# Optimization experiments

Measured on AMD Instinct MI355X. Metric: run time of the kernel, lower is better.

Reference implementation:

```python
import jax, jax.numpy as jnp
import numpy as np

NUM_ITERS = 3

def squash(s, axis=-1):
    # standard capsule squash: ||s||^2/(1+||s||^2) * s/||s||
    sq = jnp.sum(s * s, axis=axis, keepdims=True)
    norm = jnp.sqrt(sq)
    return (sq / (1.0 + sq)) * (s / norm)

def setup_inputs() -> dict:
    key = jax.random.key(0)
    kx, kw = jax.random.split(key)
    B, I, k, l, O = 512, 1152, 8, 16, 7
    x = jax.random.normal(kx, (B, I, k), dtype=jnp.float32)
    w = jax.random.normal(kw, (I, k, l, O), dtype=jnp.float32)
    return {"x": x, "w": w}

def reference(x, w):
    # x: [B, I, k]; w: [I, k, l, O]
    u_hat = jnp.einsum('BIk,IklO->BIlO', x, w)            # [B, I, l, O]
    I, _, l, _ = w.shape
    b_ij = jnp.zeros((I, l), dtype=u_hat.dtype)
    v_j = None
    for _ in range(NUM_ITERS):
        c_ij = jax.nn.softmax(b_ij, axis=0)               # softmax over I
        s_j = jnp.einsum('Il,BIlO->BlO', c_ij, u_hat)     # [B, l, O]
        v_j = jnp.transpose(squash(s_j), (0, 2, 1))       # [B, O, l]
        u_vj = jnp.einsum('BOl,BIlO->BIl', v_j, u_hat).mean(axis=0)  # [I, l]
        b_ij = b_ij + u_vj
    return v_j
```

## Files before the change

### kernel.cpp

```cpp
#include <hip/hip_runtime.h>
#include <hip/hip_bf16.h>


#define NB 512
#define NI 1152
#define NLO 112
#define NIK 9216
#define KSPLIT 96
#define SPART 57344

typedef __attribute__((ext_vector_type(8))) short bf16x8;
typedef __attribute__((ext_vector_type(4))) float f32x4;

__device__ __forceinline__ ushort f2bf(float f) {
    __hip_bfloat16 h = __float2bfloat16(f);
    return *(ushort*)&h;
}

__device__ __forceinline__ void conv_x_body(const float* __restrict__ x,
                                            ushort* __restrict__ xbf,
                                            ushort* __restrict__ xT, int bid) {
    __shared__ ushort tile[64][68];
    int kg = bid % 144, bg = bid / 144;
    int k0 = kg * 64, b0 = bg * 64;
    int t = threadIdx.x;
    for (int e = t; e < 1024; e += 256) {
        int r = e >> 4, c4 = (e & 15) * 4;
        float4 f = *(const float4*)&x[(size_t)(b0 + r) * NIK + k0 + c4];
        ushort4 u = { f2bf(f.x), f2bf(f.y), f2bf(f.z), f2bf(f.w) };
        *(ushort4*)&xbf[(size_t)(b0 + r) * NIK + k0 + c4] = u;
        tile[r][c4] = u.x; tile[r][c4 + 1] = u.y; tile[r][c4 + 2] = u.z; tile[r][c4 + 3] = u.w;
    }
    __syncthreads();
    for (int e = t; e < 1024; e += 256) {
        int kr = e >> 4, c4 = (e & 15) * 4;
        ushort4 u = { tile[c4][kr], tile[c4 + 1][kr], tile[c4 + 2][kr], tile[c4 + 3][kr] };
        *(ushort4*)&xT[(size_t)(k0 + kr) * NB + b0 + c4] = u;
    }
}

__device__ __forceinline__ void wc_tile(const float* __restrict__ cs_sh,
                                        const float* __restrict__ w,
                                        ushort* __restrict__ wcT, int ik0) {
    __shared__ ushort tile[NLO][66];
    int t = threadIdx.x;
    for (int e = t; e < 7168; e += 256) {
        int ikl = e / NLO, lo = e - ikl * NLO;
        int il = ((ikl >> 3) << 4) + lo / 7;
        tile[lo][ikl] = f2bf(cs_sh[il] * w[(size_t)(ik0 + ikl) * NLO + lo]);
    }
    __syncthreads();
    for (int e = t; e < 7168; e += 256) {
        int lo = e >> 6, ikl = e & 63;
        wcT[(size_t)lo * NIK + ik0 + ikl] = tile[lo][ikl];
    }
}

__global__ __launch_bounds__(256) void prep0(const float* __restrict__ x,
                                             ushort* __restrict__ xbf,
                                             ushort* __restrict__ xT,
                                             const float* __restrict__ w,
                                             ushort* __restrict__ wcT,
                                             float* __restrict__ Z) {
    if (blockIdx.x < 1152) { conv_x_body(x, xbf, xT, blockIdx.x); return; }
    __shared__ float cs[128];
    int t = threadIdx.x;
    if (blockIdx.x == 1152 && t < 48) Z[t] = (t < 16) ? 1.0f : 0.0f;
    if (t < 128) cs[t] = 1.0f / 1152.0f;
    __syncthreads();
    wc_tile(cs, w, wcT, (blockIdx.x - 1152) * 64);
}

__global__ __launch_bounds__(256) void wc_exp(const float* __restrict__ bijp,
                                              const float* __restrict__ w,
                                              ushort* __restrict__ wcT,
                                              float* __restrict__ Zit) {
    __shared__ float cs[128];
    int ik0 = blockIdx.x * 64;
    int t = threadIdx.x;
    if (t < 128) {
        int e = (ik0 >> 3) * 16 + t;
        cs[t] = expf(bijp[e] + bijp[e + NI * 16]);
    }
    __syncthreads();
    if (t < 16) {
        float z = 0.f;
        #pragma unroll
        for (int j = 0; j < 8; ++j) z += cs[j * 16 + t];
        atomicAdd(&Zit[t], z);
    }
    wc_tile(cs, w, wcT, ik0);
}

__global__ __launch_bounds__(256) void s_gemm(const ushort* __restrict__ xbf,
                                              const ushort* __restrict__ wcT,
                                              float* __restrict__ part) {
    int wid = blockIdx.x * 4 + (threadIdx.x >> 6);
    int lane = threadIdx.x & 63;
    int mt = wid & 31;
    int kc = wid >> 5;
    int b0 = mt * 16, k0 = kc * 96;
    int row = lane & 15, quad = lane >> 4;
    const ushort* ap = xbf + (size_t)(b0 + row) * NIK + k0 + quad * 8;
    const ushort* bp = wcT + (size_t)row * NIK + k0 + quad * 8;
    f32x4 acc[7];
    #pragma unroll
    for (int nt = 0; nt < 7; ++nt) acc[nt] = (f32x4){0.f, 0.f, 0.f, 0.f};
    #pragma unroll
    for (int ks = 0; ks < 3; ++ks) {
        bf16x8 a = *(const bf16x8*)(ap + ks * 32);
        #pragma unroll
        for (int nt = 0; nt < 7; ++nt) {
            bf16x8 bfr = *(const bf16x8*)(bp + (size_t)nt * 16 * NIK + ks * 32);
            acc[nt] = __builtin_amdgcn_mfma_f32_16x16x32_bf16(a, bfr, acc[nt], 0, 0, 0);
        }
    }
    float* pp = part + (size_t)kc * SPART + (size_t)(b0 + quad * 4) * NLO + row;
    #pragma unroll
    for (int nt = 0; nt < 7; ++nt)
        #pragma unroll
        for (int r = 0; r < 4; ++r)
            pp[(size_t)r * NLO + nt * 16] = acc[nt][r];
}

__global__ void squash_k(const float* __restrict__ part, ushort* __restrict__ vT,
                         float* __restrict__ out, const float* __restrict__ Zit,
                         int write_out) {
    int b = blockIdx.x;
    int t = threadIdx.x;
    __shared__ float sh[NLO];
    __shared__ float fac[16];
    __shared__ float zinv[16];
    if (t >= 112 && t < 128) zinv[t - 112] = 1.0f / Zit[t - 112];
    float sv = 0.f;
    if (t < NLO) {
        const float* p = part + (size_t)b * NLO + t;
        #pragma unroll 8
        for (int kc = 0; kc < KSPLIT; ++kc) sv += p[(size_t)kc * SPART];
    }
    __syncthreads();
    if (t < NLO) { sv *= zinv[t / 7]; sh[t] = sv; }
    __syncthreads();
    if (t < 16) {
        float sq = 0.f;
        #pragma unroll
        for (int o = 0; o < 7; ++o) { float e = sh[t * 7 + o]; sq += e * e; }
        fac[t] = sqrtf(sq) / (1.0f + sq);
    }
    __syncthreads();
    if (t < NLO) {
        int l = t / 7, o = t - l * 7;
        float vv = sv * fac[l];
        vT[(size_t)(o * 16 + l) * NB + b] = f2bf(vv);
        if (write_out) out[(size_t)b * NLO + o * 16 + l] = vv;
    }
}

__global__ __launch_bounds__(256) void g_fused(const ushort* __restrict__ xT,
                                               const ushort* __restrict__ vT,
                                               const float* __restrict__ w,
                                               float* __restrict__ bijp, int accum) {
    int wid = blockIdx.x * 4 + (threadIdx.x >> 6);
    int lane = threadIdx.x & 63;
    int half = wid & 1;
    int m0 = (wid >> 1) * 16;
    int kb0 = half * 256;
    int row = lane & 15, quad = lane >> 4;
    const ushort* ap = xT + (size_t)(m0 + row) * NB + kb0 + quad * 8;
    const ushort* bp = vT + (size_t)row * NB + kb0 + quad * 8;
    f32x4 acc[7];
    #pragma unroll
    for (int nt = 0; nt < 7; ++nt) acc[nt] = (f32x4){0.f, 0.f, 0.f, 0.f};
    #pragma unroll
    for (int ks = 0; ks < 8; ++ks) {
        bf16x8 a = *(const bf16x8*)(ap + ks * 32);
        #pragma unroll
        for (int nt = 0; nt < 7; ++nt) {
            bf16x8 bfr = *(const bf16x8*)(bp + (size_t)nt * 16 * NB + ks * 32);
            acc[nt] = __builtin_amdgcn_mfma_f32_16x16x32_bf16(a, bfr, acc[nt], 0, 0, 0);
        }
    }
    float S = 0.f;
    #pragma unroll
    for (int r = 0; r < 4; ++r) {
        int ik = m0 + quad * 4 + r;
        const float* wr = w + (size_t)ik * NLO + row * 7;
        float p = 0.f;
        #pragma unroll
        for (int o = 0; o < 7; ++o) p += wr[o] * acc[o][r];
        S += p;
    }
    float Sp = __shfl_down(S, 16);
    if ((quad & 1) == 0) {
        int i = (m0 >> 3) + (quad >> 1);
        float val = (S + Sp) * (1.0f / 512.0f);
        float* dst = bijp + (size_t)half * (NI * 16) + i * 16 + row;
        *dst = accum ? (*dst + val) : val;
    }
}

extern "C" void kernel_launch(void* const* d_in, const int* in_sizes, int n_in,
                              void* d_out, int out_size, void* d_ws, size_t ws_size,
                              hipStream_t stream) {
    const float* x = (const float*)d_in[0];
    const float* w = (const float*)d_in[1];
    float* out = (float*)d_out;
    float* ws = (float*)d_ws;
    float*  f_bijp = ws;
    float*  f_Z    = f_bijp + 2 * NI * 16;
    float*  f_part = f_Z + 48;
    ushort* xbf    = (ushort*)(f_part + (size_t)KSPLIT * SPART);
    ushort* xT     = xbf + (size_t)NB * NIK;
    ushort* wcT    = xT + (size_t)NIK * NB;
    ushort* vT     = wcT + (size_t)NLO * NIK;
    prep0<<<1296, 256, 0, stream>>>(x, xbf, xT, w, wcT, f_Z);
    for (int it = 0; it < 3; ++it) {
        if (it > 0) wc_exp<<<144, 256, 0, stream>>>(f_bijp, w, wcT, f_Z + it * 16);
        s_gemm<<<768, 256, 0, stream>>>(xbf, wcT, f_part);
        squash_k<<<512, 128, 0, stream>>>(f_part, vT, out, f_Z + it * 16,
                                          it == 2 ? 1 : 0);
        if (it < 2) g_fused<<<288, 256, 0, stream>>>(xT, vT, w, f_bijp, it);
    }
}
```

Before: 185.9 us.

## Fuse routing-logit update with softmax-weighted W conversion into one kernel

```diff
diff --git a/kernel.cpp b/kernel.cpp
--- a/kernel.cpp
+++ b/kernel.cpp
@@ -36,23 +36,6 @@
         int kr = e >> 4, c4 = (e & 15) * 4;
         ushort4 u = { tile[c4][kr], tile[c4 + 1][kr], tile[c4 + 2][kr], tile[c4 + 3][kr] };
         *(ushort4*)&xT[(size_t)(k0 + kr) * NB + b0 + c4] = u;
-    }
-}
-
-__device__ __forceinline__ void wc_tile(const float* __restrict__ cs_sh,
-                                        const float* __restrict__ w,
-                                        ushort* __restrict__ wcT, int ik0) {
-    __shared__ ushort tile[NLO][66];
-    int t = threadIdx.x;
-    for (int e = t; e < 7168; e += 256) {
-        int ikl = e / NLO, lo = e - ikl * NLO;
-        int il = ((ikl >> 3) << 4) + lo / 7;
-        tile[lo][ikl] = f2bf(cs_sh[il] * w[(size_t)(ik0 + ikl) * NLO + lo]);
-    }
-    __syncthreads();
-    for (int e = t; e < 7168; e += 256) {
-        int lo = e >> 6, ikl = e & 63;
-        wcT[(size_t)lo * NIK + ik0 + ikl] = tile[lo][ikl];
     }
 }
 
@@ -63,33 +46,20 @@
                                              ushort* __restrict__ wcT,
                                              float* __restrict__ Z) {
     if (blockIdx.x < 1152) { conv_x_body(x, xbf, xT, blockIdx.x); return; }
-    __shared__ float cs[128];
-    int t = threadIdx.x;
+    __shared__ ushort tile[NLO][66];
+    int t = threadIdx.x;
+    int ik0 = (blockIdx.x - 1152) * 64;
     if (blockIdx.x == 1152 && t < 48) Z[t] = (t < 16) ? 1.0f : 0.0f;
-    if (t < 128) cs[t] = 1.0f / 1152.0f;
-    __syncthreads();
-    wc_tile(cs, w, wcT, (blockIdx.x - 1152) * 64);
-}
-
-__global__ __launch_bounds__(256) void wc_exp(const float* __restrict__ bijp,
-                                              const float* __restrict__ w,
-                                              ushort* __restrict__ wcT,
-                                              float* __restrict__ Zit) {
-    __shared__ float cs[128];
-    int ik0 = blockIdx.x * 64;
-    int t = threadIdx.x;
-    if (t < 128) {
-        int e = (ik0 >> 3) * 16 + t;
-        cs[t] = expf(bijp[e] + bijp[e + NI * 16]);
-    }
-    __syncthreads();
-    if (t < 16) {
-        float z = 0.f;
-        #pragma unroll
-        for (int j = 0; j < 8; ++j) z += cs[j * 16 + t];
-        atomicAdd(&Zit[t], z);
-    }
-    wc_tile(cs, w, wcT, ik0);
+    const float cv = 1.0f / 1152.0f;
+    for (int e = t; e < 7168; e += 256) {
+        int ikl = e / NLO, lo = e - ikl * NLO;
+        tile[lo][ikl] = f2bf(cv * w[(size_t)(ik0 + ikl) * NLO + lo]);
+    }
+    __syncthreads();
+    for (int e = t; e < 7168; e += 256) {
+        int lo = e >> 6, ikl = e & 63;
+        wcT[(size_t)lo * NIK + ik0 + ikl] = tile[lo][ikl];
+    }
 }
 
 __global__ __launch_bounds__(256) void s_gemm(const ushort* __restrict__ xbf,
@@ -156,14 +126,21 @@
     }
 }
 
-__global__ __launch_bounds__(256) void g_fused(const ushort* __restrict__ xT,
-                                               const ushort* __restrict__ vT,
-                                               const float* __restrict__ w,
-                                               float* __restrict__ bijp, int accum) {
-    int wid = blockIdx.x * 4 + (threadIdx.x >> 6);
-    int lane = threadIdx.x & 63;
-    int half = wid & 1;
-    int m0 = (wid >> 1) * 16;
+__global__ __launch_bounds__(512) void g_wc(const ushort* __restrict__ xT,
+                                            const ushort* __restrict__ vT,
+                                            const float* __restrict__ w,
+                                            float* __restrict__ bij,
+                                            ushort* __restrict__ wcT,
+                                            float* __restrict__ Zit, int accum) {
+    __shared__ float bs[2][8][16];
+    __shared__ float cs[128];
+    __shared__ ushort tile[NLO][66];
+    int t = threadIdx.x;
+    int wv = t >> 6;
+    int lane = t & 63;
+    int half = wv & 1;
+    int mt = wv >> 1;
+    int m0 = blockIdx.x * 64 + mt * 16;
     int kb0 = half * 256;
     int row = lane & 15, quad = lane >> 4;
     const ushort* ap = xT + (size_t)(m0 + row) * NB + kb0 + quad * 8;
@@ -191,11 +168,34 @@
         S += p;
     }
     float Sp = __shfl_down(S, 16);
-    if ((quad & 1) == 0) {
-        int i = (m0 >> 3) + (quad >> 1);
-        float val = (S + Sp) * (1.0f / 512.0f);
-        float* dst = bijp + (size_t)half * (NI * 16) + i * 16 + row;
-        *dst = accum ? (*dst + val) : val;
+    if ((quad & 1) == 0)
+        bs[half][mt * 2 + (quad >> 1)][row] = (S + Sp) * (1.0f / 512.0f);
+    __syncthreads();
+    if (t < 128) {
+        int il = t >> 4, l = t & 15;
+        int i = blockIdx.x * 8 + il;
+        float val = bs[0][il][l] + bs[1][il][l];
+        if (accum) val += bij[i * 16 + l];
+        bij[i * 16 + l] = val;
+        cs[t] = expf(val);
+    }
+    __syncthreads();
+    if (t < 16) {
+        float z = 0.f;
+        #pragma unroll
+        for (int j = 0; j < 8; ++j) z += cs[j * 16 + t];
+        atomicAdd(&Zit[t], z);
+    }
+    int ik0 = blockIdx.x * 64;
+    for (int e = t; e < 7168; e += 512) {
+        int ikl = e / NLO, lo = e - ikl * NLO;
+        int il = ((ikl >> 3) << 4) + lo / 7;
+        tile[lo][ikl] = f2bf(cs[il] * w[(size_t)(ik0 + ikl) * NLO + lo]);
+    }
+    __syncthreads();
+    for (int e = t; e < 7168; e += 512) {
+        int lo = e >> 6, ikl = e & 63;
+        wcT[(size_t)lo * NIK + ik0 + ikl] = tile[lo][ikl];
     }
 }
 
@@ -206,8 +206,8 @@
     const float* w = (const float*)d_in[1];
     float* out = (float*)d_out;
     float* ws = (float*)d_ws;
-    float*  f_bijp = ws;
-    float*  f_Z    = f_bijp + 2 * NI * 16;
+    float*  f_bij  = ws;
+    float*  f_Z    = f_bij + NI * 16;
     float*  f_part = f_Z + 48;
     ushort* xbf    = (ushort*)(f_part + (size_t)KSPLIT * SPART);
     ushort* xT     = xbf + (size_t)NB * NIK;
@@ -215,10 +215,11 @@
     ushort* vT     = wcT + (size_t)NLO * NIK;
     prep0<<<1296, 256, 0, stream>>>(x, xbf, xT, w, wcT, f_Z);
     for (int it = 0; it < 3; ++it) {
-        if (it > 0) wc_exp<<<144, 256, 0, stream>>>(f_bijp, w, wcT, f_Z + it * 16);
         s_gemm<<<768, 256, 0, stream>>>(xbf, wcT, f_part);
         squash_k<<<512, 128, 0, stream>>>(f_part, vT, out, f_Z + it * 16,
                                           it == 2 ? 1 : 0);
-        if (it < 2) g_fused<<<288, 256, 0, stream>>>(xT, vT, w, f_bijp, it);
-    }
-}
+        if (it < 2)
+            g_wc<<<144, 512, 0, stream>>>(xT, vT, w, f_bij, wcT,
+                                          f_Z + (it + 1) * 16, it);
+    }
+}
```

Result: faster. 177.4 us (-4.6%).
